# Performance work log

Measured on AMD Instinct MI355X. Metric: run time of the kernel, lower is better.

Reference implementation:

```python
import jax, jax.numpy as jnp
import numpy as np

N = 100000   # nodes
E = 1600000  # edges
B = 64       # graphs
F = 16       # node features
H = 128      # hidden dim
G = 8        # graph features
C = 2        # classes
NGIN = 2     # extra GIN layers after the first
BN_EPS = 1e-5


def elu01(x):
    # F.elu with alpha=0.1
    return jnp.where(x > 0, x, 0.1 * jnp.expm1(x))


def batchnorm(h, gamma, beta):
    # training-mode BatchNorm1d: biased batch statistics
    mu = h.mean(axis=0)
    var = h.var(axis=0)
    return (h - mu) * jax.lax.rsqrt(var + BN_EPS) * gamma + beta


def gin_layer(x, src, dst, W1, b1, gm, bt, W2, b2):
    # GINConv eps=0: MLP(x + sum_{j->i} x_j), then ELU(0.1)
    agg = jax.ops.segment_sum(x[src], dst, num_segments=x.shape[0])
    h = (x + agg) @ W1 + b1
    h = jax.nn.relu(batchnorm(h, gm, bt))
    return elu01(h @ W2 + b2)


def setup_inputs() -> dict:
    key = jax.random.key(0)
    ks = jax.random.split(key, 24)
    s = 0.05
    inp = {
        "h0": jax.random.normal(ks[0], (N, F), jnp.float32),
        "coord0": jax.random.normal(ks[1], (N, 3), jnp.float32),
        "g0": jax.random.normal(ks[2], (B, G), jnp.float32),
        "edge_index": jax.random.randint(ks[3], (2, E), 0, N, jnp.int32),
        "batch": jnp.sort(jax.random.randint(ks[4], (N,), 0, B, jnp.int32)),
        # first GIN layer: (F+3) -> H -> H
        "w1_0": jax.random.normal(ks[5], (F + 3, H), jnp.float32) * s,
        "b1_0": jnp.zeros((H,), jnp.float32),
        "gm_0": jnp.ones((H,), jnp.float32),
        "bt_0": jnp.zeros((H,), jnp.float32),
        "w2_0": jax.random.normal(ks[6], (H, H), jnp.float32) * s,
        "b2_0": jnp.zeros((H,), jnp.float32),
        # NGIN stacked layers: H -> H -> H
        "w1_r": jax.random.normal(ks[7], (NGIN, H, H), jnp.float32) * s,
        "b1_r": jnp.zeros((NGIN, H), jnp.float32),
        "gm_r": jnp.ones((NGIN, H), jnp.float32),
        "bt_r": jnp.zeros((NGIN, H), jnp.float32),
        "w2_r": jax.random.normal(ks[8], (NGIN, H, H), jnp.float32) * s,
        "b2_r": jnp.zeros((NGIN, H), jnp.float32),
        # classifier: (2H+G) -> H -> C
        "cw1": jax.random.normal(ks[9], (2 * H + G, H), jnp.float32) * s,
        "cb1": jnp.zeros((H,), jnp.float32),
        "cgm": jnp.ones((H,), jnp.float32),
        "cbt": jnp.zeros((H,), jnp.float32),
        "cw2": jax.random.normal(ks[10], (H, C), jnp.float32) * s,
        "cb2": jnp.zeros((C,), jnp.float32),
    }
    return inp


def reference(h0, coord0, g0, edge_index, batch,
              w1_0, b1_0, gm_0, bt_0, w2_0, b2_0,
              w1_r, b1_r, gm_r, bt_r, w2_r, b2_r,
              cw1, cb1, cgm, cbt, cw2, cb2):
    src, dst = edge_index[0], edge_index[1]
    x = jnp.concatenate([h0, coord0], axis=1)  # [N, F+3]
    x = gin_layer(x, src, dst, w1_0, b1_0, gm_0, bt_0, w2_0, b2_0)
    for i in range(NGIN):
        x = gin_layer(x, src, dst, w1_r[i], b1_r[i], gm_r[i], bt_r[i], w2_r[i], b2_r[i])
    # global mean + max pooling per graph
    nb = g0.shape[0]
    cnt = jax.ops.segment_sum(jnp.ones((x.shape[0], 1), x.dtype), batch, num_segments=nb)
    mean_p = jax.ops.segment_sum(x, batch, num_segments=nb) / jnp.maximum(cnt, 1.0)
    max_p = jax.ops.segment_max(x, batch, num_segments=nb)
    pooled = jnp.concatenate([mean_p, max_p], axis=-1)  # [B, 2H]
    z = jnp.concatenate([pooled, g0], axis=1)           # [B, 2H+G]
    z = elu01(z @ cw1 + cb1)
    z = batchnorm(z, cgm, cbt)
    logits = z @ cw2 + cb2
    return jax.nn.softmax(logits, axis=1)
```

## Files before the change

### kernel.cpp

```cpp
#include <hip/hip_runtime.h>
#include <math.h>

#define NN 100000
#define EE 1600000
#define BB 64
#define FF 16
#define HH 128
#define GG 8
#define K0 19
#define BN_EPS 1e-5f
#define PCH 16
#define BSHIFT 8
#define BNODES 256
#define NBINS 391
#define BCAP 8192
#define ACH 2048
#define NB_WP 320
#define NB_X0 12500
#define STSLOT 8

typedef short bf16x8 __attribute__((ext_vector_type(8)));
typedef float f32x4 __attribute__((ext_vector_type(4)));

__device__ __forceinline__ float elu01f(float v) {
    return v > 0.f ? v : 0.1f * (__expf(v) - 1.f);
}

__device__ __forceinline__ unsigned f2bfu(float f) {
    unsigned u = __float_as_uint(f);
    unsigned r = u + 0x7FFFu + ((u >> 16) & 1u);
    return r >> 16;
}
__device__ __forceinline__ short f2bf(float f) { return (short)f2bfu(f); }
__device__ __forceinline__ float bfu2f(unsigned short b) {
    return __uint_as_float(((unsigned)b) << 16);
}
__device__ __forceinline__ float bflo(unsigned u) { return __uint_as_float(u << 16); }
__device__ __forceinline__ float bfhi(unsigned u) { return __uint_as_float(u & 0xffff0000u); }

__global__ __launch_bounds__(256) void k_binA(const int* __restrict__ esrc, const int* __restrict__ edst,
                                              int* __restrict__ bincnt, uint2* __restrict__ binbuf) {
    __shared__ int hist[NBINS];
    __shared__ int gbase[NBINS];
    __shared__ int cur[NBINS];
    __shared__ int sc[512];
    __shared__ uint2 ebuf[ACH];
    __shared__ uint2 sorted[ACH];
    int tid = threadIdx.x;
    int e0 = blockIdx.x * ACH;
    int n = min(ACH, EE - e0);
    for (int i = tid; i < NBINS; i += 256) hist[i] = 0;
    __syncthreads();
    for (int i = tid; i < n; i += 256) {
        int s = esrc[e0 + i];
        int d = edst[e0 + i];
        ebuf[i] = make_uint2((unsigned)s, (unsigned)d);
        atomicAdd(&hist[d >> BSHIFT], 1);
    }
    __syncthreads();
    sc[tid] = (tid < NBINS) ? hist[tid] : 0;
    sc[tid + 256] = (tid + 256 < NBINS) ? hist[tid + 256] : 0;
    __syncthreads();
    for (int off = 1; off < 512; off <<= 1) {
        int a0 = sc[tid], a1 = sc[tid + 256];
        int b0 = (tid >= off) ? sc[tid - off] : 0;
        int b1 = (tid + 256 >= off) ? sc[tid + 256 - off] : 0;
        __syncthreads();
        sc[tid] = a0 + b0;
        sc[tid + 256] = a1 + b1;
        __syncthreads();
    }
    for (int b = tid; b < NBINS; b += 256) {
        int c = hist[b];
        gbase[b] = (c > 0) ? atomicAdd(&bincnt[b], c) : 0;
        cur[b] = (b > 0) ? sc[b - 1] : 0;
    }
    __syncthreads();
    for (int i = tid; i < n; i += 256) {
        uint2 e = ebuf[i];
        int b = (int)(e.y >> BSHIFT);
        int pos = atomicAdd(&cur[b], 1);
        sorted[pos] = e;
    }
    __syncthreads();
    for (int i = tid; i < n; i += 256) {
        uint2 e = sorted[i];
        int b = (int)(e.y >> BSHIFT);
        int ls = (b > 0) ? sc[b - 1] : 0;
        int gpos = gbase[b] + (i - ls);
        binbuf[(size_t)b * BCAP + gpos] = e;
    }
}

__global__ __launch_bounds__(256) void k_binB(const uint2* __restrict__ binbuf, const int* __restrict__ bincnt,
                                              int* __restrict__ rp, int* __restrict__ srcs) {
    __shared__ int hist[BNODES];
    __shared__ int scx[BNODES];
    __shared__ int scur[BNODES];
    __shared__ int rsum[BNODES];
    __shared__ int sbuf[BCAP];
    int b = blockIdx.x;
    int n = bincnt[b];
    int tid = threadIdx.x;
    int v = 0;
    if (tid < b) v = bincnt[tid];
    if (tid + 256 < b) v += bincnt[tid + 256];
    rsum[tid] = v;
    hist[tid] = 0;
    __syncthreads();
    for (int off = 128; off > 0; off >>= 1) {
        if (tid < off) rsum[tid] += rsum[tid + off];
        __syncthreads();
    }
    int base = rsum[0];
    const uint2* eb = binbuf + (size_t)b * BCAP;
    for (int i = tid; i < n; i += 256)
        atomicAdd(&hist[eb[i].y & (BNODES - 1)], 1);
    __syncthreads();
    scx[tid] = hist[tid];
    __syncthreads();
    for (int off = 1; off < 256; off <<= 1) {
        int vv = (tid >= off) ? scx[tid - off] : 0;
        __syncthreads();
        scx[tid] += vv;
        __syncthreads();
    }
    int excl = (tid > 0) ? scx[tid - 1] : 0;
    int node = (b << BSHIFT) + tid;
    if (node < NN) rp[node] = base + excl;
    if (b == NBINS - 1 && tid == 0) rp[NN] = EE;
    scur[tid] = excl;
    __syncthreads();
    for (int i = tid; i < n; i += 256) {
        uint2 e = eb[i];
        int pos = atomicAdd(&scur[e.y & (BNODES - 1)], 1);
        sbuf[pos] = (int)e.x;
    }
    __syncthreads();
    for (int i = tid; i < n; i += 256) srcs[base + i] = sbuf[i];
}

__global__ __launch_bounds__(256) void k_prep(const float* __restrict__ w2_0, const float* __restrict__ w1_r,
                                              const float* __restrict__ w2_r, short* __restrict__ wt,
                                              const float* __restrict__ h0, const float* __restrict__ coord,
                                              unsigned short* __restrict__ x0,
                                              const int* __restrict__ batch, int* __restrict__ gptr) {
    int b = blockIdx.x;
    int tid = threadIdx.x;
    if (b == 0 && tid <= BB) {
        int t = tid;
        int lo = 0, hi = NN;
        while (lo < hi) { int mid = (lo + hi) >> 1; if (batch[mid] < t) lo = mid + 1; else hi = mid; }
        gptr[t] = lo;
    }
    if (b < NB_WP) {
        int t = b * 256 + tid;
        if (t >= 5 * HH * HH) return;
        int m = t >> 14;
        int rem = t & 16383;
        int col = rem >> 7;
        int k = rem & 127;
        const float* src = (m == 0) ? w2_0 : (m <= 2 ? w1_r + (size_t)(m - 1) * HH * HH
                                                     : w2_r + (size_t)(m - 3) * HH * HH);
        wt[t] = f2bf(src[k * HH + col]);
    } else {
        int i = (b - NB_WP) * 256 + tid;
        if (i >= NN * 32) return;
        int node = i >> 5, k = i & 31;
        float v = 0.f;
        if (k < FF) v = h0[node * FF + k];
        else if (k < K0) v = coord[node * 3 + (k - FF)];
        x0[i] = (unsigned short)f2bfu(v);
    }
}

__global__ __launch_bounds__(256) void k_agg_small(const uint4* __restrict__ x, const int* __restrict__ rp,
                                                   const int* __restrict__ srcs, float* __restrict__ y) {
    int w = (blockIdx.x * 256 + threadIdx.x) >> 6;
    int lane = threadIdx.x & 63;
    if (w >= NN) return;
    int e = lane >> 2, q = lane & 3;
    int beg = rp[w], end = rp[w + 1];
    float acc[8];
    {
        if (e == 0) {
            uint4 u = x[(size_t)w * 4 + q];
            acc[0] = bflo(u.x); acc[1] = bfhi(u.x);
            acc[2] = bflo(u.y); acc[3] = bfhi(u.y);
            acc[4] = bflo(u.z); acc[5] = bfhi(u.z);
            acc[6] = bflo(u.w); acc[7] = bfhi(u.w);
        } else {
            #pragma unroll
            for (int j = 0; j < 8; j++) acc[j] = 0.f;
        }
    }
    for (int p = beg; p < end; p += 16) {
        int rem = end - p;
        bool act = e < rem;
        int sn = act ? srcs[p + e] : 0;
        uint4 u = x[(size_t)sn * 4 + q];
        float m = act ? 1.f : 0.f;
        acc[0] = fmaf(m, bflo(u.x), acc[0]); acc[1] = fmaf(m, bfhi(u.x), acc[1]);
        acc[2] = fmaf(m, bflo(u.y), acc[2]); acc[3] = fmaf(m, bfhi(u.y), acc[3]);
        acc[4] = fmaf(m, bflo(u.z), acc[4]); acc[5] = fmaf(m, bfhi(u.z), acc[5]);
        acc[6] = fmaf(m, bflo(u.w), acc[6]); acc[7] = fmaf(m, bfhi(u.w), acc[7]);
    }
    #pragma unroll
    for (int mask = 4; mask <= 32; mask <<= 1)
        #pragma unroll
        for (int j = 0; j < 8; j++)
            acc[j] += __shfl_xor(acc[j], mask, 64);
    if (e == 0) {
        float4* yo = (float4*)(y + (size_t)w * 32 + q * 8);
        yo[0] = make_float4(acc[0], acc[1], acc[2], acc[3]);
        yo[1] = make_float4(acc[4], acc[5], acc[6], acc[7]);
    }
}

template<int K>
__global__ __launch_bounds__(256) void k_gemm_small(const float* __restrict__ in,
        const float* __restrict__ W, const float* __restrict__ bias,
        unsigned short* __restrict__ out, float* __restrict__ gstat) {
    constexpr int SK = ((K + 3) / 4) * 4 + 4;
    __shared__ __align__(16) float yt[32 * SK];
    __shared__ float red[256];
    int tid = threadIdx.x;
    int row0 = blockIdx.x * 32;
    for (int t = tid; t < 32 * SK; t += 256) {
        int r = t / SK, k = t - r * SK;
        float v = 0.f;
        if (k < K) v = in[(size_t)(row0 + r) * 32 + k];
        yt[t] = v;
    }
    __syncthreads();
    int col = tid & 127;
    int rg = tid >> 7;
    float acc[16];
    #pragma unroll
    for (int r = 0; r < 16; r++) acc[r] = 0.f;
    const float* ybase = &yt[rg * 16 * SK];
    int kk = 0;
    for (; kk + 4 <= K; kk += 4) {
        float w0 = W[(kk + 0) * HH + col];
        float w1 = W[(kk + 1) * HH + col];
        float w2 = W[(kk + 2) * HH + col];
        float w3 = W[(kk + 3) * HH + col];
        #pragma unroll
        for (int r = 0; r < 16; r++) {
            const float4 v = *(const float4*)&ybase[r * SK + kk];
            acc[r] = fmaf(v.x, w0, acc[r]);
            acc[r] = fmaf(v.y, w1, acc[r]);
            acc[r] = fmaf(v.z, w2, acc[r]);
            acc[r] = fmaf(v.w, w3, acc[r]);
        }
    }
    if constexpr (K % 4 != 0) {
        float w[4];
        #pragma unroll
        for (int j = 0; j < 4; j++) w[j] = (kk + j < K) ? W[(kk + j) * HH + col] : 0.f;
        #pragma unroll
        for (int r = 0; r < 16; r++) {
            const float4 v = *(const float4*)&ybase[r * SK + kk];
            acc[r] = fmaf(v.x, w[0], acc[r]);
            acc[r] = fmaf(v.y, w[1], acc[r]);
            acc[r] = fmaf(v.z, w[2], acc[r]);
            acc[r] = fmaf(v.w, w[3], acc[r]);
        }
    }
    float bcol = bias[col];
    float s = 0.f, s2 = 0.f;
    #pragma unroll
    for (int r = 0; r < 16; r++) {
        float hv = acc[r] + bcol;
        out[(size_t)(row0 + rg * 16 + r) * HH + col] = (unsigned short)f2bfu(hv);
        s += hv; s2 = fmaf(hv, hv, s2);
    }
    int sl = (blockIdx.x & (STSLOT - 1)) << 8;
    red[tid] = s; __syncthreads();
    if (tid < 128) atomicAdd(&gstat[sl + tid], s + red[tid + 128]);
    __syncthreads();
    red[tid] = s2; __syncthreads();
    if (tid < 128) atomicAdd(&gstat[sl + 128 + tid], s2 + red[tid + 128]);
}

__global__ __launch_bounds__(256) void k_agg128_bf(const uint4* __restrict__ x4, const int* __restrict__ rp,
                                                   const int* __restrict__ srcs, uint4* __restrict__ y4) {
    int wave = (blockIdx.x * 256 + threadIdx.x) >> 6;
    int lane = threadIdx.x & 63;
    int g = lane >> 4, il = lane & 15;
    int w = wave * 4 + g;
    if (w >= NN) return;
    int beg = rp[w], end = rp[w + 1];
    uint4 u = x4[(size_t)w * 16 + il];
    float a0 = bflo(u.x), a1 = bfhi(u.x), a2 = bflo(u.y), a3 = bfhi(u.y);
    float a4 = bflo(u.z), a5 = bfhi(u.z), a6 = bflo(u.w), a7 = bfhi(u.w);
    float b0 = 0.f, b1 = 0.f, b2 = 0.f, b3 = 0.f, b4 = 0.f, b5 = 0.f, b6 = 0.f, b7 = 0.f;
    int p = beg;
    for (; p + 8 <= end; p += 8) {
        int s0 = srcs[p + 0], s1 = srcs[p + 1], s2 = srcs[p + 2], s3 = srcs[p + 3];
        int s4 = srcs[p + 4], s5 = srcs[p + 5], s6 = srcs[p + 6], s7 = srcs[p + 7];
        uint4 u0 = x4[(size_t)s0 * 16 + il];
        uint4 u1 = x4[(size_t)s1 * 16 + il];
        uint4 u2 = x4[(size_t)s2 * 16 + il];
        uint4 u3 = x4[(size_t)s3 * 16 + il];
        uint4 u4 = x4[(size_t)s4 * 16 + il];
        uint4 u5 = x4[(size_t)s5 * 16 + il];
        uint4 u6 = x4[(size_t)s6 * 16 + il];
        uint4 u7 = x4[(size_t)s7 * 16 + il];
        a0 += (bflo(u0.x) + bflo(u1.x)) + (bflo(u2.x) + bflo(u3.x));
        a1 += (bfhi(u0.x) + bfhi(u1.x)) + (bfhi(u2.x) + bfhi(u3.x));
        a2 += (bflo(u0.y) + bflo(u1.y)) + (bflo(u2.y) + bflo(u3.y));
        a3 += (bfhi(u0.y) + bfhi(u1.y)) + (bfhi(u2.y) + bfhi(u3.y));
        a4 += (bflo(u0.z) + bflo(u1.z)) + (bflo(u2.z) + bflo(u3.z));
        a5 += (bfhi(u0.z) + bfhi(u1.z)) + (bfhi(u2.z) + bfhi(u3.z));
        a6 += (bflo(u0.w) + bflo(u1.w)) + (bflo(u2.w) + bflo(u3.w));
        a7 += (bfhi(u0.w) + bfhi(u1.w)) + (bfhi(u2.w) + bfhi(u3.w));
        b0 += (bflo(u4.x) + bflo(u5.x)) + (bflo(u6.x) + bflo(u7.x));
        b1 += (bfhi(u4.x) + bfhi(u5.x)) + (bfhi(u6.x) + bfhi(u7.x));
        b2 += (bflo(u4.y) + bflo(u5.y)) + (bflo(u6.y) + bflo(u7.y));
        b3 += (bfhi(u4.y) + bfhi(u5.y)) + (bfhi(u6.y) + bfhi(u7.y));
        b4 += (bflo(u4.z) + bflo(u5.z)) + (bflo(u6.z) + bflo(u7.z));
        b5 += (bfhi(u4.z) + bfhi(u5.z)) + (bfhi(u6.z) + bfhi(u7.z));
        b6 += (bflo(u4.w) + bflo(u5.w)) + (bflo(u6.w) + bflo(u7.w));
        b7 += (bfhi(u4.w) + bfhi(u5.w)) + (bfhi(u6.w) + bfhi(u7.w));
    }
    for (; p + 4 <= end; p += 4) {
        int s0 = srcs[p + 0], s1 = srcs[p + 1], s2 = srcs[p + 2], s3 = srcs[p + 3];
        uint4 u0 = x4[(size_t)s0 * 16 + il];
        uint4 u1 = x4[(size_t)s1 * 16 + il];
        uint4 u2 = x4[(size_t)s2 * 16 + il];
        uint4 u3 = x4[(size_t)s3 * 16 + il];
        a0 += (bflo(u0.x) + bflo(u1.x)) + (bflo(u2.x) + bflo(u3.x));
        a1 += (bfhi(u0.x) + bfhi(u1.x)) + (bfhi(u2.x) + bfhi(u3.x));
        a2 += (bflo(u0.y) + bflo(u1.y)) + (bflo(u2.y) + bflo(u3.y));
        a3 += (bfhi(u0.y) + bfhi(u1.y)) + (bfhi(u2.y) + bfhi(u3.y));
        a4 += (bflo(u0.z) + bflo(u1.z)) + (bflo(u2.z) + bflo(u3.z));
        a5 += (bfhi(u0.z) + bfhi(u1.z)) + (bfhi(u2.z) + bfhi(u3.z));
        a6 += (bflo(u0.w) + bflo(u1.w)) + (bflo(u2.w) + bflo(u3.w));
        a7 += (bfhi(u0.w) + bfhi(u1.w)) + (bfhi(u2.w) + bfhi(u3.w));
    }
    for (; p < end; ++p) {
        uint4 uu = x4[(size_t)srcs[p] * 16 + il];
        a0 += bflo(uu.x); a1 += bfhi(uu.x);
        a2 += bflo(uu.y); a3 += bfhi(uu.y);
        a4 += bflo(uu.z); a5 += bfhi(uu.z);
        a6 += bflo(uu.w); a7 += bfhi(uu.w);
    }
    a0 += b0; a1 += b1; a2 += b2; a3 += b3;
    a4 += b4; a5 += b5; a6 += b6; a7 += b7;
    uint4 o;
    o.x = f2bfu(a0) | (f2bfu(a1) << 16);
    o.y = f2bfu(a2) | (f2bfu(a3) << 16);
    o.z = f2bfu(a4) | (f2bfu(a5) << 16);
    o.w = f2bfu(a6) | (f2bfu(a7) << 16);
    y4[(size_t)w * 16 + il] = o;
}

__global__ __launch_bounds__(256) void k_gemm_s1(const unsigned short* __restrict__ in,
        const short* __restrict__ WT, const float* __restrict__ bias,
        unsigned short* __restrict__ out, float* __restrict__ gstat) {
    __shared__ __align__(16) short Al[64 * 136];
    __shared__ float lsum[HH], lsq[HH];
    int tid = threadIdx.x;
    if (tid < HH) { lsum[tid] = 0.f; lsq[tid] = 0.f; }
    int row0 = blockIdx.x * 64;
    {
        int r = tid >> 2;
        int k0 = (tid & 3) * 32;
        int grow = row0 + r;
        uint4* d4 = (uint4*)&Al[r * 136 + k0];
        if (grow < NN) {
            const uint4* s4 = (const uint4*)(in + (size_t)grow * HH + k0);
            d4[0] = s4[0]; d4[1] = s4[1]; d4[2] = s4[2]; d4[3] = s4[3];
        } else {
            uint4 z = {0, 0, 0, 0};
            d4[0] = z; d4[1] = z; d4[2] = z; d4[3] = z;
        }
    }
    __syncthreads();
    int wave = tid >> 6;
    int lane = tid & 63;
    int ln = lane & 15, quad = lane >> 4;
    int wcol0 = wave * 32;
    f32x4 acc[4][2];
    #pragma unroll
    for (int rt = 0; rt < 4; rt++)
        #pragma unroll
        for (int ct = 0; ct < 2; ct++) acc[rt][ct] = (f32x4){0.f, 0.f, 0.f, 0.f};
    #pragma unroll
    for (int ks = 0; ks < 4; ks++) {
        bf16x8 a[4], b[2];
        #pragma unroll
        for (int ct = 0; ct < 2; ct++)
            b[ct] = *(const bf16x8*)(WT + (size_t)(wcol0 + ct * 16 + ln) * HH + ks * 32 + quad * 8);
        #pragma unroll
        for (int rt = 0; rt < 4; rt++)
            a[rt] = *(const bf16x8*)(&Al[(rt * 16 + ln) * 136 + ks * 32 + quad * 8]);
        #pragma unroll
        for (int rt = 0; rt < 4; rt++)
            #pragma unroll
            for (int ct = 0; ct < 2; ct++)
                acc[rt][ct] = __builtin_amdgcn_mfma_f32_16x16x32_bf16(a[rt], b[ct], acc[rt][ct], 0, 0, 0);
    }
    float b0 = bias[wcol0 + ln];
    float b1 = bias[wcol0 + 16 + ln];
    float s[2] = {0.f, 0.f}, s2[2] = {0.f, 0.f};
    #pragma unroll
    for (int rt = 0; rt < 4; rt++) {
        #pragma unroll
        for (int r = 0; r < 4; r++) {
            int grow = row0 + rt * 16 + quad * 4 + r;
            if (grow < NN) {
                float hv0 = acc[rt][0][r] + b0;
                float hv1 = acc[rt][1][r] + b1;
                out[(size_t)grow * HH + wcol0 + ln] = (unsigned short)f2bfu(hv0);
                out[(size_t)grow * HH + wcol0 + 16 + ln] = (unsigned short)f2bfu(hv1);
                s[0] += hv0; s2[0] = fmaf(hv0, hv0, s2[0]);
                s[1] += hv1; s2[1] = fmaf(hv1, hv1, s2[1]);
            }
        }
    }
    atomicAdd(&lsum[wcol0 + ln], s[0]);
    atomicAdd(&lsum[wcol0 + 16 + ln], s[1]);
    atomicAdd(&lsq[wcol0 + ln], s2[0]);
    atomicAdd(&lsq[wcol0 + 16 + ln], s2[1]);
    __syncthreads();
    if (tid < HH) {
        int sl = (blockIdx.x & (STSLOT - 1)) << 8;
        atomicAdd(&gstat[sl + tid], lsum[tid]);
        atomicAdd(&gstat[sl + 128 + tid], lsq[tid]);
    }
}

__global__ __launch_bounds__(256) void k_gemm_bn(const unsigned short* __restrict__ in,
        const short* __restrict__ WT, const float* __restrict__ bias,
        const float* __restrict__ gstat, const float* __restrict__ gm, const float* __restrict__ bt,
        unsigned short* __restrict__ out) {
    __shared__ __align__(16) short Al[64 * 136];
    __shared__ __align__(16) float bnsc[HH], bnsh[HH];
    int tid = threadIdx.x;
    if (tid < HH) {
        float s = 0.f, s2 = 0.f;
        #pragma unroll
        for (int k = 0; k < STSLOT; ++k) {
            s += gstat[(k << 8) + tid];
            s2 += gstat[(k << 8) + 128 + tid];
        }
        float mu = s * (1.f / NN);
        float var = fmaxf(s2 * (1.f / NN) - mu * mu, 0.f);
        float a = gm[tid] * rsqrtf(var + BN_EPS);
        bnsc[tid] = a;
        bnsh[tid] = fmaf(-mu, a, bt[tid]);
    }
    __syncthreads();
    int row0 = blockIdx.x * 64;
    {
        int r = tid >> 2;
        int k0 = (tid & 3) * 32;
        int grow = row0 + r;
        short* dst = &Al[r * 136 + k0];
        if (grow < NN) {
            const uint4* s4 = (const uint4*)(in + (size_t)grow * HH + k0);
            unsigned* d = (unsigned*)dst;
            #pragma unroll
            for (int q = 0; q < 4; q++) {
                uint4 u = s4[q];
                float4 sc0 = *(const float4*)(bnsc + k0 + q * 8);
                float4 sh0 = *(const float4*)(bnsh + k0 + q * 8);
                float4 sc1 = *(const float4*)(bnsc + k0 + q * 8 + 4);
                float4 sh1 = *(const float4*)(bnsh + k0 + q * 8 + 4);
                float a0 = bflo(u.x), a1 = bfhi(u.x);
                float a2 = bflo(u.y), a3 = bfhi(u.y);
                float a4 = bflo(u.z), a5 = bfhi(u.z);
                float a6 = bflo(u.w), a7 = bfhi(u.w);
                a0 = fmaxf(fmaf(a0, sc0.x, sh0.x), 0.f);
                a1 = fmaxf(fmaf(a1, sc0.y, sh0.y), 0.f);
                a2 = fmaxf(fmaf(a2, sc0.z, sh0.z), 0.f);
                a3 = fmaxf(fmaf(a3, sc0.w, sh0.w), 0.f);
                a4 = fmaxf(fmaf(a4, sc1.x, sh1.x), 0.f);
                a5 = fmaxf(fmaf(a5, sc1.y, sh1.y), 0.f);
                a6 = fmaxf(fmaf(a6, sc1.z, sh1.z), 0.f);
                a7 = fmaxf(fmaf(a7, sc1.w, sh1.w), 0.f);
                d[q * 4 + 0] = f2bfu(a0) | (f2bfu(a1) << 16);
                d[q * 4 + 1] = f2bfu(a2) | (f2bfu(a3) << 16);
                d[q * 4 + 2] = f2bfu(a4) | (f2bfu(a5) << 16);
                d[q * 4 + 3] = f2bfu(a6) | (f2bfu(a7) << 16);
            }
        } else {
            uint4 z = {0, 0, 0, 0};
            uint4* d4 = (uint4*)dst;
            d4[0] = z; d4[1] = z; d4[2] = z; d4[3] = z;
        }
    }
    __syncthreads();
    int wave = tid >> 6;
    int lane = tid & 63;
    int ln = lane & 15, quad = lane >> 4;
    int wcol0 = wave * 32;
    f32x4 acc[4][2];
    #pragma unroll
    for (int rt = 0; rt < 4; rt++)
        #pragma unroll
        for (int ct = 0; ct < 2; ct++) acc[rt][ct] = (f32x4){0.f, 0.f, 0.f, 0.f};
    #pragma unroll
    for (int ks = 0; ks < 4; ks++) {
        bf16x8 a[4], b[2];
        #pragma unroll
        for (int ct = 0; ct < 2; ct++)
            b[ct] = *(const bf16x8*)(WT + (size_t)(wcol0 + ct * 16 + ln) * HH + ks * 32 + quad * 8);
        #pragma unroll
        for (int rt = 0; rt < 4; rt++)
            a[rt] = *(const bf16x8*)(&Al[(rt * 16 + ln) * 136 + ks * 32 + quad * 8]);
        #pragma unroll
        for (int rt = 0; rt < 4; rt++)
            #pragma unroll
            for (int ct = 0; ct < 2; ct++)
                acc[rt][ct] = __builtin_amdgcn_mfma_f32_16x16x32_bf16(a[rt], b[ct], acc[rt][ct], 0, 0, 0);
    }
    float b0 = bias[wcol0 + ln];
    float b1 = bias[wcol0 + 16 + ln];
    #pragma unroll
    for (int rt = 0; rt < 4; rt++) {
        #pragma unroll
        for (int r = 0; r < 4; r++) {
            int grow = row0 + rt * 16 + quad * 4 + r;
            if (grow < NN) {
                float hv0 = elu01f(acc[rt][0][r] + b0);
                float hv1 = elu01f(acc[rt][1][r] + b1);
                out[(size_t)grow * HH + wcol0 + ln] = (unsigned short)f2bfu(hv0);
                out[(size_t)grow * HH + wcol0 + 16 + ln] = (unsigned short)f2bfu(hv1);
            }
        }
    }
}

__global__ __launch_bounds__(128) void k_pool_part(const unsigned short* __restrict__ x,
                                                   const int* __restrict__ gptr,
                                                   float* __restrict__ psum, float* __restrict__ pmax) {
    int g = blockIdx.x >> 4;
    int ch = blockIdx.x & 15;
    int s = gptr[g], e = gptr[g + 1];
    int len = e - s;
    int per = (len + PCH - 1) / PCH;
    int lo = s + ch * per;
    int hi = min(lo + per, e);
    int c = threadIdx.x;
    float sm = 0.f, mx = -INFINITY;
    for (int i = lo; i < hi; ++i) {
        float v = bfu2f(x[(size_t)i * HH + c]);
        sm += v; mx = fmaxf(mx, v);
    }
    psum[(size_t)blockIdx.x * HH + c] = sm;
    pmax[(size_t)blockIdx.x * HH + c] = mx;
}

__global__ __launch_bounds__(128) void k_pool_cls1(const float* __restrict__ psum, const float* __restrict__ pmax,
                                                   const int* __restrict__ gptr, const float* __restrict__ g0,
                                                   const float* __restrict__ cw1, const float* __restrict__ cb1,
                                                   float* __restrict__ z1) {
    __shared__ float zr[264];
    int g = blockIdx.x, c = threadIdx.x;
    float sm = 0.f, mx = -INFINITY;
    for (int ch = 0; ch < PCH; ++ch) {
        sm += psum[(size_t)(g * PCH + ch) * HH + c];
        mx = fmaxf(mx, pmax[(size_t)(g * PCH + ch) * HH + c]);
    }
    int cntn = gptr[g + 1] - gptr[g];
    zr[c] = sm / (float)max(cntn, 1);
    zr[128 + c] = mx;
    if (c < GG) zr[256 + c] = g0[g * GG + c];
    __syncthreads();
    float acc = cb1[c];
    for (int k = 0; k < 264; ++k) acc = fmaf(zr[k], cw1[k * HH + c], acc);
    z1[g * HH + c] = elu01f(acc);
}

__global__ __launch_bounds__(128) void k_cls2(const float* __restrict__ z1, const float* __restrict__ cgm,
                                              const float* __restrict__ cbt, const float* __restrict__ cw2,
                                              const float* __restrict__ cb2, float* __restrict__ outp) {
    __shared__ float zn[HH * 65];
    int c = threadIdx.x;
    float s = 0.f, s2 = 0.f;
    for (int g = 0; g < BB; ++g) {
        float v = z1[g * HH + c];
        s += v; s2 = fmaf(v, v, s2);
    }
    float mu = s * (1.f / BB);
    float var = fmaxf(s2 * (1.f / BB) - mu * mu, 0.f);
    float a = cgm[c] * rsqrtf(var + BN_EPS);
    float sh = fmaf(-mu, a, cbt[c]);
    for (int g = 0; g < BB; ++g) zn[c * 65 + g] = fmaf(z1[g * HH + c], a, sh);
    __syncthreads();
    if (c < BB) {
        float l0 = cb2[0], l1 = cb2[1];
        for (int k = 0; k < HH; ++k) {
            float v = zn[k * 65 + c];
            l0 = fmaf(v, cw2[k * 2 + 0], l0);
            l1 = fmaf(v, cw2[k * 2 + 1], l1);
        }
        float m = fmaxf(l0, l1);
        float e0 = __expf(l0 - m), e1 = __expf(l1 - m);
        float inv = 1.f / (e0 + e1);
        outp[c * 2 + 0] = e0 * inv;
        outp[c * 2 + 1] = e1 * inv;
    }
}

extern "C" void kernel_launch(void* const* d_in, const int* in_sizes, int n_in,
                              void* d_out, int out_size, void* d_ws, size_t ws_size,
                              hipStream_t stream) {
    (void)in_sizes; (void)n_in; (void)out_size; (void)ws_size;
    const float* h0     = (const float*)d_in[0];
    const float* coord0 = (const float*)d_in[1];
    const float* g0     = (const float*)d_in[2];
    const int*   eidx   = (const int*)d_in[3];
    const int*   batch  = (const int*)d_in[4];
    const float* w1_0   = (const float*)d_in[5];
    const float* b1_0   = (const float*)d_in[6];
    const float* gm_0   = (const float*)d_in[7];
    const float* bt_0   = (const float*)d_in[8];
    const float* w2_0   = (const float*)d_in[9];
    const float* b2_0   = (const float*)d_in[10];
    const float* w1_r   = (const float*)d_in[11];
    const float* b1_r   = (const float*)d_in[12];
    const float* gm_r   = (const float*)d_in[13];
    const float* bt_r   = (const float*)d_in[14];
    const float* w2_r   = (const float*)d_in[15];
    const float* b2_r   = (const float*)d_in[16];
    const float* cw1    = (const float*)d_in[17];
    const float* cb1    = (const float*)d_in[18];
    const float* cgm    = (const float*)d_in[19];
    const float* cbt    = (const float*)d_in[20];
    const float* cw2    = (const float*)d_in[21];
    const float* cb2    = (const float*)d_in[22];
    float* outp = (float*)d_out;

    const int* esrc = eidx;
    const int* edst = eidx + EE;

    char* p = (char*)d_ws;
    auto alloc = [&](size_t bytes) { void* r = (void*)p; p += (bytes + 255) & ~(size_t)255; return r; };
    int*            bincnt   = (int*)alloc((size_t)NBINS * 4);
    float*          gstat    = (float*)alloc((size_t)3 * STSLOT * 256 * 4);
    unsigned short* x0bf     = (unsigned short*)alloc((size_t)NN * 32 * 2);
    float*          y19f     = (float*)alloc((size_t)NN * 32 * 4);
    unsigned short* hbf      = (unsigned short*)alloc((size_t)NN * HH * 2);
    unsigned*       xbf      = (unsigned*)alloc((size_t)NN * 64 * 4);
    unsigned*       ybf      = (unsigned*)alloc((size_t)NN * 64 * 4);
    int*            rp       = (int*)alloc((size_t)(NN + 1) * 4);
    int*            srcs     = (int*)alloc((size_t)EE * 4);
    int*            gptr     = (int*)alloc((BB + 1) * 4);
    short*          wt       = (short*)alloc((size_t)5 * HH * HH * 2);
    float*          psum     = (float*)alloc((size_t)BB * PCH * HH * 4);
    float*          pmax     = (float*)alloc((size_t)BB * PCH * HH * 4);
    float*          z1b      = (float*)alloc((size_t)BB * HH * 4);
    uint2*          binbuf   = (uint2*)alloc((size_t)NBINS * BCAP * 8);

    const int NB_A = (EE + ACH - 1) / ACH;
    const int NB_AGG = (NN * 64 + 255) / 256;
    const int NB_AGG4 = (NN + 15) / 16;
    const int NB_G32 = NN / 32;
    const int NB_G64 = (NN + 63) / 64;

    size_t zlen = (size_t)((char*)x0bf - (char*)bincnt);
    hipMemsetAsync(bincnt, 0, zlen, stream);

    k_binA<<<NB_A, 256, 0, stream>>>(esrc, edst, bincnt, binbuf);
    k_binB<<<NBINS, 256, 0, stream>>>(binbuf, bincnt, rp, srcs);
    k_prep<<<NB_WP + NB_X0, 256, 0, stream>>>(w2_0, w1_r, w2_r, wt, h0, coord0, x0bf, batch, gptr);

    k_agg_small<<<NB_AGG, 256, 0, stream>>>((const uint4*)x0bf, rp, srcs, y19f);
    k_gemm_small<K0><<<NB_G32, 256, 0, stream>>>(y19f, w1_0, b1_0, hbf, gstat);
    k_gemm_bn<<<NB_G64, 256, 0, stream>>>(hbf, wt, b2_0, gstat, gm_0, bt_0, (unsigned short*)xbf);

    for (int i = 0; i < 2; ++i) {
        float* gs = gstat + (size_t)(1 + i) * STSLOT * 256;
        k_agg128_bf<<<NB_AGG4, 256, 0, stream>>>((const uint4*)xbf, rp, srcs, (uint4*)ybf);
        k_gemm_s1<<<NB_G64, 256, 0, stream>>>((const unsigned short*)ybf,
                wt + (size_t)(1 + i) * HH * HH, b1_r + i * HH, hbf, gs);
        k_gemm_bn<<<NB_G64, 256, 0, stream>>>(hbf, wt + (size_t)(3 + i) * HH * HH, b2_r + i * HH,
                                              gs, gm_r + i * HH, bt_r + i * HH, (unsigned short*)xbf);
    }

    k_pool_part<<<BB * PCH, 128, 0, stream>>>((const unsigned short*)xbf, gptr, psum, pmax);
    k_pool_cls1<<<BB, 128, 0, stream>>>(psum, pmax, gptr, g0, cw1, cb1, z1b);
    k_cls2<<<1, 128, 0, stream>>>(z1b, cgm, cbt, cw2, cb2, outp);
}
```

Baseline: 496.0 us.

## Fuse neighbor aggregation into first GEMM of GIN layers via shared memory

The separate 128-wide gather/sum kernel and the first MLP GEMM are merged. Each block aggregates its 64 rows straight into the LDS tile that feeds the MFMA GEMM, so the intermediate aggregated buffer is never written to or read back from global memory, and one launch per layer goes away. In exchange, each block now runs a long, latency-bound gather phase before its MFMA phase, and each wave serially handles 4 row groups. That may reduce the parallelism available to hide gather latency compared with the standalone aggregation kernel.

Result: slower. 531.9 us (+7.2%).

```diff
diff --git a/kernel.cpp b/kernel.cpp
--- a/kernel.cpp
+++ b/kernel.cpp
@@ -283,103 +283,88 @@
     if (tid < 128) atomicAdd(&gstat[sl + 128 + tid], s2 + red[tid + 128]);
 }
 
-__global__ __launch_bounds__(256) void k_agg128_bf(const uint4* __restrict__ x4, const int* __restrict__ rp,
-                                                   const int* __restrict__ srcs, uint4* __restrict__ y4) {
-    int wave = (blockIdx.x * 256 + threadIdx.x) >> 6;
-    int lane = threadIdx.x & 63;
-    int g = lane >> 4, il = lane & 15;
-    int w = wave * 4 + g;
-    if (w >= NN) return;
-    int beg = rp[w], end = rp[w + 1];
-    uint4 u = x4[(size_t)w * 16 + il];
-    float a0 = bflo(u.x), a1 = bfhi(u.x), a2 = bflo(u.y), a3 = bfhi(u.y);
-    float a4 = bflo(u.z), a5 = bfhi(u.z), a6 = bflo(u.w), a7 = bfhi(u.w);
-    float b0 = 0.f, b1 = 0.f, b2 = 0.f, b3 = 0.f, b4 = 0.f, b5 = 0.f, b6 = 0.f, b7 = 0.f;
-    int p = beg;
-    for (; p + 8 <= end; p += 8) {
-        int s0 = srcs[p + 0], s1 = srcs[p + 1], s2 = srcs[p + 2], s3 = srcs[p + 3];
-        int s4 = srcs[p + 4], s5 = srcs[p + 5], s6 = srcs[p + 6], s7 = srcs[p + 7];
-        uint4 u0 = x4[(size_t)s0 * 16 + il];
-        uint4 u1 = x4[(size_t)s1 * 16 + il];
-        uint4 u2 = x4[(size_t)s2 * 16 + il];
-        uint4 u3 = x4[(size_t)s3 * 16 + il];
-        uint4 u4 = x4[(size_t)s4 * 16 + il];
-        uint4 u5 = x4[(size_t)s5 * 16 + il];
-        uint4 u6 = x4[(size_t)s6 * 16 + il];
-        uint4 u7 = x4[(size_t)s7 * 16 + il];
-        a0 += (bflo(u0.x) + bflo(u1.x)) + (bflo(u2.x) + bflo(u3.x));
-        a1 += (bfhi(u0.x) + bfhi(u1.x)) + (bfhi(u2.x) + bfhi(u3.x));
-        a2 += (bflo(u0.y) + bflo(u1.y)) + (bflo(u2.y) + bflo(u3.y));
-        a3 += (bfhi(u0.y) + bfhi(u1.y)) + (bfhi(u2.y) + bfhi(u3.y));
-        a4 += (bflo(u0.z) + bflo(u1.z)) + (bflo(u2.z) + bflo(u3.z));
-        a5 += (bfhi(u0.z) + bfhi(u1.z)) + (bfhi(u2.z) + bfhi(u3.z));
-        a6 += (bflo(u0.w) + bflo(u1.w)) + (bflo(u2.w) + bflo(u3.w));
-        a7 += (bfhi(u0.w) + bfhi(u1.w)) + (bfhi(u2.w) + bfhi(u3.w));
-        b0 += (bflo(u4.x) + bflo(u5.x)) + (bflo(u6.x) + bflo(u7.x));
-        b1 += (bfhi(u4.x) + bfhi(u5.x)) + (bfhi(u6.x) + bfhi(u7.x));
-        b2 += (bflo(u4.y) + bflo(u5.y)) + (bflo(u6.y) + bflo(u7.y));
-        b3 += (bfhi(u4.y) + bfhi(u5.y)) + (bfhi(u6.y) + bfhi(u7.y));
-        b4 += (bflo(u4.z) + bflo(u5.z)) + (bflo(u6.z) + bflo(u7.z));
-        b5 += (bfhi(u4.z) + bfhi(u5.z)) + (bfhi(u6.z) + bfhi(u7.z));
-        b6 += (bflo(u4.w) + bflo(u5.w)) + (bflo(u6.w) + bflo(u7.w));
-        b7 += (bfhi(u4.w) + bfhi(u5.w)) + (bfhi(u6.w) + bfhi(u7.w));
-    }
-    for (; p + 4 <= end; p += 4) {
-        int s0 = srcs[p + 0], s1 = srcs[p + 1], s2 = srcs[p + 2], s3 = srcs[p + 3];
-        uint4 u0 = x4[(size_t)s0 * 16 + il];
-        uint4 u1 = x4[(size_t)s1 * 16 + il];
-        uint4 u2 = x4[(size_t)s2 * 16 + il];
-        uint4 u3 = x4[(size_t)s3 * 16 + il];
-        a0 += (bflo(u0.x) + bflo(u1.x)) + (bflo(u2.x) + bflo(u3.x));
-        a1 += (bfhi(u0.x) + bfhi(u1.x)) + (bfhi(u2.x) + bfhi(u3.x));
-        a2 += (bflo(u0.y) + bflo(u1.y)) + (bflo(u2.y) + bflo(u3.y));
-        a3 += (bfhi(u0.y) + bfhi(u1.y)) + (bfhi(u2.y) + bfhi(u3.y));
-        a4 += (bflo(u0.z) + bflo(u1.z)) + (bflo(u2.z) + bflo(u3.z));
-        a5 += (bfhi(u0.z) + bfhi(u1.z)) + (bfhi(u2.z) + bfhi(u3.z));
-        a6 += (bflo(u0.w) + bflo(u1.w)) + (bflo(u2.w) + bflo(u3.w));
-        a7 += (bfhi(u0.w) + bfhi(u1.w)) + (bfhi(u2.w) + bfhi(u3.w));
-    }
-    for (; p < end; ++p) {
-        uint4 uu = x4[(size_t)srcs[p] * 16 + il];
-        a0 += bflo(uu.x); a1 += bfhi(uu.x);
-        a2 += bflo(uu.y); a3 += bfhi(uu.y);
-        a4 += bflo(uu.z); a5 += bfhi(uu.z);
-        a6 += bflo(uu.w); a7 += bfhi(uu.w);
-    }
-    a0 += b0; a1 += b1; a2 += b2; a3 += b3;
-    a4 += b4; a5 += b5; a6 += b6; a7 += b7;
-    uint4 o;
-    o.x = f2bfu(a0) | (f2bfu(a1) << 16);
-    o.y = f2bfu(a2) | (f2bfu(a3) << 16);
-    o.z = f2bfu(a4) | (f2bfu(a5) << 16);
-    o.w = f2bfu(a6) | (f2bfu(a7) << 16);
-    y4[(size_t)w * 16 + il] = o;
-}
-
-__global__ __launch_bounds__(256) void k_gemm_s1(const unsigned short* __restrict__ in,
-        const short* __restrict__ WT, const float* __restrict__ bias,
+__global__ __launch_bounds__(256) void k_agg_gemm(const uint4* __restrict__ x4, const int* __restrict__ rp,
+        const int* __restrict__ srcs, const short* __restrict__ WT, const float* __restrict__ bias,
         unsigned short* __restrict__ out, float* __restrict__ gstat) {
     __shared__ __align__(16) short Al[64 * 136];
     __shared__ float lsum[HH], lsq[HH];
     int tid = threadIdx.x;
+    int wave = tid >> 6, lane = tid & 63;
+    int g = lane >> 4, il = lane & 15;
     if (tid < HH) { lsum[tid] = 0.f; lsq[tid] = 0.f; }
     int row0 = blockIdx.x * 64;
-    {
-        int r = tid >> 2;
-        int k0 = (tid & 3) * 32;
-        int grow = row0 + r;
-        uint4* d4 = (uint4*)&Al[r * 136 + k0];
-        if (grow < NN) {
-            const uint4* s4 = (const uint4*)(in + (size_t)grow * HH + k0);
-            d4[0] = s4[0]; d4[1] = s4[1]; d4[2] = s4[2]; d4[3] = s4[3];
-        } else {
-            uint4 z = {0, 0, 0, 0};
-            d4[0] = z; d4[1] = z; d4[2] = z; d4[3] = z;
-        }
-    }
-    __syncthreads();
-    int wave = tid >> 6;
-    int lane = tid & 63;
+    for (int it = 0; it < 4; ++it) {
+        int r = wave * 16 + it * 4 + g;
+        int w = row0 + r;
+        float a0 = 0.f, a1 = 0.f, a2 = 0.f, a3 = 0.f, a4 = 0.f, a5 = 0.f, a6 = 0.f, a7 = 0.f;
+        float b0 = 0.f, b1 = 0.f, b2 = 0.f, b3 = 0.f, b4 = 0.f, b5 = 0.f, b6 = 0.f, b7 = 0.f;
+        if (w < NN) {
+            uint4 u = x4[(size_t)w * 16 + il];
+            a0 = bflo(u.x); a1 = bfhi(u.x); a2 = bflo(u.y); a3 = bfhi(u.y);
+            a4 = bflo(u.z); a5 = bfhi(u.z); a6 = bflo(u.w); a7 = bfhi(u.w);
+            int beg = rp[w], end = rp[w + 1];
+            int p = beg;
+            for (; p + 8 <= end; p += 8) {
+                int s0 = srcs[p + 0], s1 = srcs[p + 1], s2 = srcs[p + 2], s3 = srcs[p + 3];
+                int s4 = srcs[p + 4], s5 = srcs[p + 5], s6 = srcs[p + 6], s7 = srcs[p + 7];
+                uint4 u0 = x4[(size_t)s0 * 16 + il];
+                uint4 u1 = x4[(size_t)s1 * 16 + il];
+                uint4 u2 = x4[(size_t)s2 * 16 + il];
+                uint4 u3 = x4[(size_t)s3 * 16 + il];
+                uint4 u4 = x4[(size_t)s4 * 16 + il];
+                uint4 u5 = x4[(size_t)s5 * 16 + il];
+                uint4 u6 = x4[(size_t)s6 * 16 + il];
+                uint4 u7 = x4[(size_t)s7 * 16 + il];
+                a0 += (bflo(u0.x) + bflo(u1.x)) + (bflo(u2.x) + bflo(u3.x));
+                a1 += (bfhi(u0.x) + bfhi(u1.x)) + (bfhi(u2.x) + bfhi(u3.x));
+                a2 += (bflo(u0.y) + bflo(u1.y)) + (bflo(u2.y) + bflo(u3.y));
+                a3 += (bfhi(u0.y) + bfhi(u1.y)) + (bfhi(u2.y) + bfhi(u3.y));
+                a4 += (bflo(u0.z) + bflo(u1.z)) + (bflo(u2.z) + bflo(u3.z));
+                a5 += (bfhi(u0.z) + bfhi(u1.z)) + (bfhi(u2.z) + bfhi(u3.z));
+                a6 += (bflo(u0.w) + bflo(u1.w)) + (bflo(u2.w) + bflo(u3.w));
+                a7 += (bfhi(u0.w) + bfhi(u1.w)) + (bfhi(u2.w) + bfhi(u3.w));
+                b0 += (bflo(u4.x) + bflo(u5.x)) + (bflo(u6.x) + bflo(u7.x));
+                b1 += (bfhi(u4.x) + bfhi(u5.x)) + (bfhi(u6.x) + bfhi(u7.x));
+                b2 += (bflo(u4.y) + bflo(u5.y)) + (bflo(u6.y) + bflo(u7.y));
+                b3 += (bfhi(u4.y) + bfhi(u5.y)) + (bfhi(u6.y) + bfhi(u7.y));
+                b4 += (bflo(u4.z) + bflo(u5.z)) + (bflo(u6.z) + bflo(u7.z));
+                b5 += (bfhi(u4.z) + bfhi(u5.z)) + (bfhi(u6.z) + bfhi(u7.z));
+                b6 += (bflo(u4.w) + bflo(u5.w)) + (bflo(u6.w) + bflo(u7.w));
+                b7 += (bfhi(u4.w) + bfhi(u5.w)) + (bfhi(u6.w) + bfhi(u7.w));
+            }
+            for (; p + 4 <= end; p += 4) {
+                int s0 = srcs[p + 0], s1 = srcs[p + 1], s2 = srcs[p + 2], s3 = srcs[p + 3];
+                uint4 u0 = x4[(size_t)s0 * 16 + il];
+                uint4 u1 = x4[(size_t)s1 * 16 + il];
+                uint4 u2 = x4[(size_t)s2 * 16 + il];
+                uint4 u3 = x4[(size_t)s3 * 16 + il];
+                a0 += (bflo(u0.x) + bflo(u1.x)) + (bflo(u2.x) + bflo(u3.x));
+                a1 += (bfhi(u0.x) + bfhi(u1.x)) + (bfhi(u2.x) + bfhi(u3.x));
+                a2 += (bflo(u0.y) + bflo(u1.y)) + (bflo(u2.y) + bflo(u3.y));
+                a3 += (bfhi(u0.y) + bfhi(u1.y)) + (bfhi(u2.y) + bfhi(u3.y));
+                a4 += (bflo(u0.z) + bflo(u1.z)) + (bflo(u2.z) + bflo(u3.z));
+                a5 += (bfhi(u0.z) + bfhi(u1.z)) + (bfhi(u2.z) + bfhi(u3.z));
+                a6 += (bflo(u0.w) + bflo(u1.w)) + (bflo(u2.w) + bflo(u3.w));
+                a7 += (bfhi(u0.w) + bfhi(u1.w)) + (bfhi(u2.w) + bfhi(u3.w));
+            }
+            for (; p < end; ++p) {
+                uint4 uu = x4[(size_t)srcs[p] * 16 + il];
+                a0 += bflo(uu.x); a1 += bfhi(uu.x);
+                a2 += bflo(uu.y); a3 += bfhi(uu.y);
+                a4 += bflo(uu.z); a5 += bfhi(uu.z);
+                a6 += bflo(uu.w); a7 += bfhi(uu.w);
+            }
+        }
+        a0 += b0; a1 += b1; a2 += b2; a3 += b3;
+        a4 += b4; a5 += b5; a6 += b6; a7 += b7;
+        uint4 o;
+        o.x = f2bfu(a0) | (f2bfu(a1) << 16);
+        o.y = f2bfu(a2) | (f2bfu(a3) << 16);
+        o.z = f2bfu(a4) | (f2bfu(a5) << 16);
+        o.w = f2bfu(a6) | (f2bfu(a7) << 16);
+        *(uint4*)&Al[r * 136 + il * 8] = o;
+    }
+    __syncthreads();
     int ln = lane & 15, quad = lane >> 4;
     int wcol0 = wave * 32;
     f32x4 acc[4][2];
@@ -402,8 +387,8 @@
             for (int ct = 0; ct < 2; ct++)
                 acc[rt][ct] = __builtin_amdgcn_mfma_f32_16x16x32_bf16(a[rt], b[ct], acc[rt][ct], 0, 0, 0);
     }
-    float b0 = bias[wcol0 + ln];
-    float b1 = bias[wcol0 + 16 + ln];
+    float bi0 = bias[wcol0 + ln];
+    float bi1 = bias[wcol0 + 16 + ln];
     float s[2] = {0.f, 0.f}, s2[2] = {0.f, 0.f};
     #pragma unroll
     for (int rt = 0; rt < 4; rt++) {
@@ -411,8 +396,8 @@
         for (int r = 0; r < 4; r++) {
             int grow = row0 + rt * 16 + quad * 4 + r;
             if (grow < NN) {
-                float hv0 = acc[rt][0][r] + b0;
-                float hv1 = acc[rt][1][r] + b1;
+                float hv0 = acc[rt][0][r] + bi0;
+                float hv1 = acc[rt][1][r] + bi1;
                 out[(size_t)grow * HH + wcol0 + ln] = (unsigned short)f2bfu(hv0);
                 out[(size_t)grow * HH + wcol0 + 16 + ln] = (unsigned short)f2bfu(hv1);
                 s[0] += hv0; s2[0] = fmaf(hv0, hv0, s2[0]);
@@ -646,7 +631,6 @@
     float*          y19f     = (float*)alloc((size_t)NN * 32 * 4);
     unsigned short* hbf      = (unsigned short*)alloc((size_t)NN * HH * 2);
     unsigned*       xbf      = (unsigned*)alloc((size_t)NN * 64 * 4);
-    unsigned*       ybf      = (unsigned*)alloc((size_t)NN * 64 * 4);
     int*            rp       = (int*)alloc((size_t)(NN + 1) * 4);
     int*            srcs     = (int*)alloc((size_t)EE * 4);
     int*            gptr     = (int*)alloc((BB + 1) * 4);
@@ -658,7 +642,6 @@
 
     const int NB_A = (EE + ACH - 1) / ACH;
     const int NB_AGG = (NN * 64 + 255) / 256;
-    const int NB_AGG4 = (NN + 15) / 16;
     const int NB_G32 = NN / 32;
     const int NB_G64 = (NN + 63) / 64;
 
@@ -675,8 +658,7 @@
 
     for (int i = 0; i < 2; ++i) {
         float* gs = gstat + (size_t)(1 + i) * STSLOT * 256;
-        k_agg128_bf<<<NB_AGG4, 256, 0, stream>>>((const uint4*)xbf, rp, srcs, (uint4*)ybf);
-        k_gemm_s1<<<NB_G64, 256, 0, stream>>>((const unsigned short*)ybf,
+        k_agg_gemm<<<NB_G64, 256, 0, stream>>>((const uint4*)xbf, rp, srcs,
                 wt + (size_t)(1 + i) * HH * HH, b1_r + i * HH, hbf, gs);
         k_gemm_bn<<<NB_G64, 256, 0, stream>>>(hbf, wt + (size_t)(3 + i) * HH * HH, b2_r + i * HH,
                                               gs, gm_r + i * HH, bt_r + i * HH, (unsigned short*)xbf);
```

## Replace two-pass binned CSR build with degree count, scan, and atomic scatter

Applied to the files above, without the earlier changes.

The CSR construction moves from a two-pass shared-memory bin sort (k_binA/k_binB with a large binbuf staging buffer) to three kernels. The first counts per-node degree with global atomics, the second scans to build row pointers, and the third scatters source ids using per-node atomic cursors. This removes the staging buffer traffic and the heavy shared-memory sorting. In exchange it relies on 1.6M global atomics on random addresses, twice over, and the order of neighbours within a row becomes nondeterministic, which can change floating-point summation order.

After: 655.0 us. 32.1% more time.

```diff
diff --git a/kernel.cpp b/kernel.cpp
--- a/kernel.cpp
+++ b/kernel.cpp
@@ -13,7 +13,6 @@
 #define BSHIFT 8
 #define BNODES 256
 #define NBINS 391
-#define BCAP 8192
 #define ACH 2048
 #define NB_WP 320
 #define NB_X0 12500
@@ -38,86 +37,41 @@
 __device__ __forceinline__ float bflo(unsigned u) { return __uint_as_float(u << 16); }
 __device__ __forceinline__ float bfhi(unsigned u) { return __uint_as_float(u & 0xffff0000u); }
 
-__global__ __launch_bounds__(256) void k_binA(const int* __restrict__ esrc, const int* __restrict__ edst,
-                                              int* __restrict__ bincnt, uint2* __restrict__ binbuf) {
+__global__ __launch_bounds__(256) void k_deg(const int* __restrict__ edst,
+                                             int* __restrict__ deg, int* __restrict__ bincnt) {
     __shared__ int hist[NBINS];
-    __shared__ int gbase[NBINS];
-    __shared__ int cur[NBINS];
-    __shared__ int sc[512];
-    __shared__ uint2 ebuf[ACH];
-    __shared__ uint2 sorted[ACH];
     int tid = threadIdx.x;
     int e0 = blockIdx.x * ACH;
     int n = min(ACH, EE - e0);
     for (int i = tid; i < NBINS; i += 256) hist[i] = 0;
     __syncthreads();
     for (int i = tid; i < n; i += 256) {
-        int s = esrc[e0 + i];
         int d = edst[e0 + i];
-        ebuf[i] = make_uint2((unsigned)s, (unsigned)d);
+        atomicAdd(&deg[d], 1);
         atomicAdd(&hist[d >> BSHIFT], 1);
     }
     __syncthreads();
-    sc[tid] = (tid < NBINS) ? hist[tid] : 0;
-    sc[tid + 256] = (tid + 256 < NBINS) ? hist[tid + 256] : 0;
-    __syncthreads();
-    for (int off = 1; off < 512; off <<= 1) {
-        int a0 = sc[tid], a1 = sc[tid + 256];
-        int b0 = (tid >= off) ? sc[tid - off] : 0;
-        int b1 = (tid + 256 >= off) ? sc[tid + 256 - off] : 0;
-        __syncthreads();
-        sc[tid] = a0 + b0;
-        sc[tid + 256] = a1 + b1;
-        __syncthreads();
-    }
-    for (int b = tid; b < NBINS; b += 256) {
-        int c = hist[b];
-        gbase[b] = (c > 0) ? atomicAdd(&bincnt[b], c) : 0;
-        cur[b] = (b > 0) ? sc[b - 1] : 0;
-    }
-    __syncthreads();
-    for (int i = tid; i < n; i += 256) {
-        uint2 e = ebuf[i];
-        int b = (int)(e.y >> BSHIFT);
-        int pos = atomicAdd(&cur[b], 1);
-        sorted[pos] = e;
-    }
-    __syncthreads();
-    for (int i = tid; i < n; i += 256) {
-        uint2 e = sorted[i];
-        int b = (int)(e.y >> BSHIFT);
-        int ls = (b > 0) ? sc[b - 1] : 0;
-        int gpos = gbase[b] + (i - ls);
-        binbuf[(size_t)b * BCAP + gpos] = e;
-    }
-}
-
-__global__ __launch_bounds__(256) void k_binB(const uint2* __restrict__ binbuf, const int* __restrict__ bincnt,
-                                              int* __restrict__ rp, int* __restrict__ srcs) {
-    __shared__ int hist[BNODES];
-    __shared__ int scx[BNODES];
-    __shared__ int scur[BNODES];
-    __shared__ int rsum[BNODES];
-    __shared__ int sbuf[BCAP];
-    int b = blockIdx.x;
-    int n = bincnt[b];
-    int tid = threadIdx.x;
+    for (int i = tid; i < NBINS; i += 256)
+        if (hist[i]) atomicAdd(&bincnt[i], hist[i]);
+}
+
+__global__ __launch_bounds__(256) void k_scan(const int* __restrict__ deg, const int* __restrict__ bincnt,
+                                              int* __restrict__ rp, int* __restrict__ cur) {
+    __shared__ int rsum[256];
+    __shared__ int scx[256];
+    int b = blockIdx.x, tid = threadIdx.x;
     int v = 0;
     if (tid < b) v = bincnt[tid];
     if (tid + 256 < b) v += bincnt[tid + 256];
     rsum[tid] = v;
-    hist[tid] = 0;
     __syncthreads();
     for (int off = 128; off > 0; off >>= 1) {
         if (tid < off) rsum[tid] += rsum[tid + off];
         __syncthreads();
     }
     int base = rsum[0];
-    const uint2* eb = binbuf + (size_t)b * BCAP;
-    for (int i = tid; i < n; i += 256)
-        atomicAdd(&hist[eb[i].y & (BNODES - 1)], 1);
-    __syncthreads();
-    scx[tid] = hist[tid];
+    int node = (b << BSHIFT) + tid;
+    scx[tid] = (node < NN) ? deg[node] : 0;
     __syncthreads();
     for (int off = 1; off < 256; off <<= 1) {
         int vv = (tid >= off) ? scx[tid - off] : 0;
@@ -126,18 +80,17 @@
         __syncthreads();
     }
     int excl = (tid > 0) ? scx[tid - 1] : 0;
-    int node = (b << BSHIFT) + tid;
-    if (node < NN) rp[node] = base + excl;
+    if (node < NN) { rp[node] = base + excl; cur[node] = base + excl; }
     if (b == NBINS - 1 && tid == 0) rp[NN] = EE;
-    scur[tid] = excl;
-    __syncthreads();
-    for (int i = tid; i < n; i += 256) {
-        uint2 e = eb[i];
-        int pos = atomicAdd(&scur[e.y & (BNODES - 1)], 1);
-        sbuf[pos] = (int)e.x;
-    }
-    __syncthreads();
-    for (int i = tid; i < n; i += 256) srcs[base + i] = sbuf[i];
+}
+
+__global__ __launch_bounds__(256) void k_scatter(const int* __restrict__ esrc, const int* __restrict__ edst,
+                                                 int* __restrict__ cur, int* __restrict__ srcs) {
+    int i = blockIdx.x * 256 + threadIdx.x;
+    if (i >= EE) return;
+    int d = edst[i];
+    int pos = atomicAdd(&cur[d], 1);
+    srcs[pos] = esrc[i];
 }
 
 __global__ __launch_bounds__(256) void k_prep(const float* __restrict__ w2_0, const float* __restrict__ w1_r,
@@ -642,21 +595,23 @@
     auto alloc = [&](size_t bytes) { void* r = (void*)p; p += (bytes + 255) & ~(size_t)255; return r; };
     int*            bincnt   = (int*)alloc((size_t)NBINS * 4);
     float*          gstat    = (float*)alloc((size_t)3 * STSLOT * 256 * 4);
+    int*            deg      = (int*)alloc((size_t)NN * 4);
     unsigned short* x0bf     = (unsigned short*)alloc((size_t)NN * 32 * 2);
     float*          y19f     = (float*)alloc((size_t)NN * 32 * 4);
     unsigned short* hbf      = (unsigned short*)alloc((size_t)NN * HH * 2);
     unsigned*       xbf      = (unsigned*)alloc((size_t)NN * 64 * 4);
     unsigned*       ybf      = (unsigned*)alloc((size_t)NN * 64 * 4);
     int*            rp       = (int*)alloc((size_t)(NN + 1) * 4);
+    int*            cur      = (int*)alloc((size_t)NN * 4);
     int*            srcs     = (int*)alloc((size_t)EE * 4);
     int*            gptr     = (int*)alloc((BB + 1) * 4);
     short*          wt       = (short*)alloc((size_t)5 * HH * HH * 2);
     float*          psum     = (float*)alloc((size_t)BB * PCH * HH * 4);
     float*          pmax     = (float*)alloc((size_t)BB * PCH * HH * 4);
     float*          z1b      = (float*)alloc((size_t)BB * HH * 4);
-    uint2*          binbuf   = (uint2*)alloc((size_t)NBINS * BCAP * 8);
-
-    const int NB_A = (EE + ACH - 1) / ACH;
+
+    const int NB_DEG = (EE + ACH - 1) / ACH;
+    const int NB_SCAT = (EE + 255) / 256;
     const int NB_AGG = (NN * 64 + 255) / 256;
     const int NB_AGG4 = (NN + 15) / 16;
     const int NB_G32 = NN / 32;
@@ -665,8 +620,9 @@
     size_t zlen = (size_t)((char*)x0bf - (char*)bincnt);
     hipMemsetAsync(bincnt, 0, zlen, stream);
 
-    k_binA<<<NB_A, 256, 0, stream>>>(esrc, edst, bincnt, binbuf);
-    k_binB<<<NBINS, 256, 0, stream>>>(binbuf, bincnt, rp, srcs);
+    k_deg<<<NB_DEG, 256, 0, stream>>>(edst, deg, bincnt);
+    k_scan<<<NBINS, 256, 0, stream>>>(deg, bincnt, rp, cur);
+    k_scatter<<<NB_SCAT, 256, 0, stream>>>(esrc, edst, cur, srcs);
     k_prep<<<NB_WP + NB_X0, 256, 0, stream>>>(w2_0, w1_r, w2_r, wt, h0, coord0, x0bf, batch, gptr);
 
     k_agg_small<<<NB_AGG, 256, 0, stream>>>((const uint4*)x0bf, rp, srcs, y19f);
```
